# Kernel optimization log

Hardware: AMD Instinct MI355X
Metric: run time of the kernel (lower is better)

Reference implementation:

```python
import jax, jax.numpy as jnp
import numpy as np

B, S, D = 1, 2048, 4096
H, KVH, HD = 32, 8, 128


def setup_inputs() -> dict:
    key = jax.random.key(0)
    ks = jax.random.split(key, 6)
    x = jax.random.normal(ks[0], (B, S, D), dtype=jnp.float32)
    # Llama3 RoPE angles: theta = 500000
    inv_freq = 1.0 / (500000.0 ** (np.arange(0, HD, 2, dtype=np.float32) / HD))
    ang = np.arange(S, dtype=np.float32)[:, None] * inv_freq[None, :]  # [S, HD//2]
    freqs_cos = jnp.asarray(np.cos(ang), dtype=jnp.float32)
    freqs_sin = jnp.asarray(np.sin(ang), dtype=jnp.float32)
    sc = 0.02
    wq = jax.random.normal(ks[1], (H * HD, D), dtype=jnp.float32) * sc
    wk = jax.random.normal(ks[2], (KVH * HD, D), dtype=jnp.float32) * sc
    wv = jax.random.normal(ks[3], (KVH * HD, D), dtype=jnp.float32) * sc
    wo = jax.random.normal(ks[4], (D, H * HD), dtype=jnp.float32) * sc
    return {"x": x, "freqs_cos": freqs_cos, "freqs_sin": freqs_sin,
            "wq": wq, "wk": wk, "wv": wv, "wo": wo}


def _rope(t, cos, sin):
    # t: [B, S, h, HD]; rotate consecutive pairs (complex multiply)
    t2 = t.reshape(*t.shape[:-1], HD // 2, 2)
    x0, x1 = t2[..., 0], t2[..., 1]
    c = cos[None, :, None, :]
    s = sin[None, :, None, :]
    r0 = x0 * c - x1 * s
    r1 = x0 * s + x1 * c
    return jnp.stack([r0, r1], axis=-1).reshape(t.shape)


def reference(x, freqs_cos, freqs_sin, wq, wk, wv, wo):
    b, s, _ = x.shape
    q = jnp.einsum('bsd,ed->bse', x, wq).reshape(b, s, H, HD)
    k = jnp.einsum('bsd,ed->bse', x, wk).reshape(b, s, KVH, HD)
    v = jnp.einsum('bsd,ed->bse', x, wv).reshape(b, s, KVH, HD)
    q = _rope(q, freqs_cos, freqs_sin)
    k = _rope(k, freqs_cos, freqs_sin)
    # GQA: repeat kv heads
    rep = H // KVH
    k = jnp.repeat(k, rep, axis=2)
    v = jnp.repeat(v, rep, axis=2)
    scale = 1.0 / jnp.sqrt(jnp.asarray(HD, dtype=x.dtype))
    scores = jnp.einsum('bqhd,bkhd->bhqk', q, k) * scale
    causal = jnp.tril(jnp.ones((s, s), dtype=bool))
    scores = jnp.where(causal[None, None], scores, jnp.finfo(scores.dtype).min)
    p = jax.nn.softmax(scores, axis=-1)
    out = jnp.einsum('bhqk,bkhd->bqhd', p, v).reshape(b, s, H * HD)
    return jnp.einsum('bse,de->bsd', out, wo)
```

## Files before the change

### kernel.cpp

```cpp
#include <hip/hip_runtime.h>

typedef unsigned short u16;
typedef short bf16x8 __attribute__((ext_vector_type(8)));
typedef float f32x4 __attribute__((ext_vector_type(4)));

#define S_LEN 2048
#define ATT_SCALE 0.08838834764831845f
#define NEG_BIG  -1.0e30f

static __device__ __forceinline__ float bf2f(u16 u) {
  union { unsigned int i; float f; } v; v.i = ((unsigned int)u) << 16; return v.f;
}
static __device__ __forceinline__ u16 f2bf(float f) {
  union { float f; unsigned int i; } v; v.f = f;
  unsigned int x = v.i;
  return (u16)((x + 0x7fffu + ((x >> 16) & 1u)) >> 16);
}

static __device__ __forceinline__ void gl_lds16(const u16* g, u16* l) {
  __builtin_amdgcn_global_load_lds(
      (const __attribute__((address_space(1))) unsigned int*)g,
      (__attribute__((address_space(3))) unsigned int*)l, 16, 0, 0);
}

static __device__ __forceinline__ bf16x8 load8(const u16* p) { return *(const bf16x8*)p; }
static __device__ __forceinline__ bf16x8 load8(const float* p) {
  f32x4 a = *(const f32x4*)p;
  f32x4 b = *(const f32x4*)(p + 4);
  bf16x8 r;
  r[0] = (short)f2bf(a[0]); r[1] = (short)f2bf(a[1]);
  r[2] = (short)f2bf(a[2]); r[3] = (short)f2bf(a[3]);
  r[4] = (short)f2bf(b[0]); r[5] = (short)f2bf(b[1]);
  r[6] = (short)f2bf(b[2]); r[7] = (short)f2bf(b[3]);
  return r;
}
static __device__ __forceinline__ void store_out(u16* C, size_t i, float v)  { C[i] = f2bf(v); }
static __device__ __forceinline__ void store_out(float* C, size_t i, float v){ C[i] = v; }

__global__ __launch_bounds__(256) void f2b_kernel(
    const float* __restrict__ s, u16* __restrict__ d, int n8) {
  int i = blockIdx.x * 256 + threadIdx.x;
  if (i >= n8) return;
  *(bf16x8*)&d[(size_t)i * 8] = load8(s + (size_t)i * 8);
}

template <typename OT>
static __device__ __forceinline__ void gemm_core(
    const u16* __restrict__ A, const u16* __restrict__ B, OT* __restrict__ C,
    int K, int ldc, int bm, int bn) {
  __shared__ __align__(16) u16 As[128 * 64];
  __shared__ __align__(16) u16 Bs[128 * 64];
  const int tid  = threadIdx.x;
  const int lane = tid & 63;
  const int wave = tid >> 6;
  const int wm = (wave >> 1) << 6;
  const int wn = (wave & 1) << 6;
  const int col  = lane & 15;
  const int quad = lane >> 4;

  const f32x4 fzero = {0.f, 0.f, 0.f, 0.f};
  f32x4 acc[4][4];
#pragma unroll
  for (int i = 0; i < 4; ++i)
#pragma unroll
    for (int j = 0; j < 4; ++j) acc[i][j] = fzero;

  const int srow = (lane >> 3);
  const int sc8  = lane & 7;

  for (int k0 = 0; k0 < K; k0 += 64) {
#pragma unroll
    for (int i = 0; i < 4; ++i) {
      int r = wave * 32 + i * 8 + srow;
      int src = (sc8 ^ (r & 7)) << 3;
      gl_lds16(A + (size_t)(bm + r) * K + k0 + src, &As[(wave * 32 + i * 8) * 64]);
      gl_lds16(B + (size_t)(bn + r) * K + k0 + src, &Bs[(wave * 32 + i * 8) * 64]);
    }
    __syncthreads();
#pragma unroll
    for (int kk = 0; kk < 64; kk += 32) {
      bf16x8 af[4], bfr[4];
#pragma unroll
      for (int mt = 0; mt < 4; ++mt) {
        int row = wm + mt * 16 + col;
        af[mt] = *(const bf16x8*)&As[row * 64 + ((((kk >> 3) + quad) ^ (col & 7)) << 3)];
      }
#pragma unroll
      for (int nt = 0; nt < 4; ++nt) {
        int row = wn + nt * 16 + col;
        bfr[nt] = *(const bf16x8*)&Bs[row * 64 + ((((kk >> 3) + quad) ^ (col & 7)) << 3)];
      }
#pragma unroll
      for (int mt = 0; mt < 4; ++mt)
#pragma unroll
        for (int nt = 0; nt < 4; ++nt)
          acc[mt][nt] = __builtin_amdgcn_mfma_f32_16x16x32_bf16(
              af[mt], bfr[nt], acc[mt][nt], 0, 0, 0);
    }
    __syncthreads();
  }
#pragma unroll
  for (int mt = 0; mt < 4; ++mt)
#pragma unroll
    for (int nt = 0; nt < 4; ++nt)
#pragma unroll
      for (int r = 0; r < 4; ++r) {
        int row = bm + wm + mt * 16 + quad * 4 + r;
        int cn  = bn + wn + nt * 16 + col;
        store_out(C, (size_t)row * ldc + cn, acc[mt][nt][r]);
      }
}

__global__ __launch_bounds__(256) void gemm_qkv(
    const u16* __restrict__ xb, const u16* __restrict__ wqb,
    const u16* __restrict__ wkb, const u16* __restrict__ wvb,
    u16* __restrict__ q, u16* __restrict__ k, u16* __restrict__ v) {
  int bx = blockIdx.x;
  const u16* B; u16* C; int ldc, bn;
  if (bx < 32)      { B = wqb; C = q; ldc = 4096; bn = bx * 128; }
  else if (bx < 40) { B = wkb; C = k; ldc = 1024; bn = (bx - 32) * 128; }
  else              { B = wvb; C = v; ldc = 1024; bn = (bx - 40) * 128; }
  gemm_core<u16>(xb, B, C, 4096, ldc, blockIdx.y * 128, bn);
}

__global__ __launch_bounds__(256) void gemm_o(
    const u16* __restrict__ ao, const u16* __restrict__ wob, float* __restrict__ out) {
  gemm_core<float>(ao, wob, out, 4096, 4096, blockIdx.y * 128, blockIdx.x * 128);
}

#define LDK 72
template <typename AT, typename BT, typename OT>
__global__ __launch_bounds__(256) void gemm_bt(
    const AT* __restrict__ A, const BT* __restrict__ B,
    OT* __restrict__ C, int M, int N, int K) {
  __shared__ __align__(16) u16 As[128 * LDK];
  __shared__ __align__(16) u16 Bs[128 * LDK];
  const int tid  = threadIdx.x;
  const int lane = tid & 63;
  const int wave = tid >> 6;
  const int wm = (wave >> 1) << 6;
  const int wn = (wave & 1) << 6;
  const int col  = lane & 15;
  const int quad = lane >> 4;
  const int bm = blockIdx.y * 128;
  const int bn = blockIdx.x * 128;

  const f32x4 fzero = {0.f, 0.f, 0.f, 0.f};
  f32x4 acc[4][4];
#pragma unroll
  for (int i = 0; i < 4; ++i)
#pragma unroll
    for (int j = 0; j < 4; ++j) acc[i][j] = fzero;

  const int sr = tid >> 3;
  const int sc = (tid & 7) * 8;
  const AT* Aptr = A + (size_t)(bm + sr) * K + sc;
  const BT* Bptr = B + (size_t)(bn + sr) * K + sc;

  for (int k0 = 0; k0 < K; k0 += 64) {
#pragma unroll
    for (int p = 0; p < 4; ++p) {
      *(bf16x8*)&As[(sr + 32 * p) * LDK + sc] = load8(Aptr + (size_t)(32 * p) * K + k0);
      *(bf16x8*)&Bs[(sr + 32 * p) * LDK + sc] = load8(Bptr + (size_t)(32 * p) * K + k0);
    }
    __syncthreads();
#pragma unroll
    for (int kk = 0; kk < 64; kk += 32) {
      bf16x8 af[4], bfr[4];
#pragma unroll
      for (int mt = 0; mt < 4; ++mt)
        af[mt] = *(const bf16x8*)&As[(wm + mt * 16 + col) * LDK + kk + quad * 8];
#pragma unroll
      for (int nt = 0; nt < 4; ++nt)
        bfr[nt] = *(const bf16x8*)&Bs[(wn + nt * 16 + col) * LDK + kk + quad * 8];
#pragma unroll
      for (int mt = 0; mt < 4; ++mt)
#pragma unroll
        for (int nt = 0; nt < 4; ++nt)
          acc[mt][nt] = __builtin_amdgcn_mfma_f32_16x16x32_bf16(
              af[mt], bfr[nt], acc[mt][nt], 0, 0, 0);
    }
    __syncthreads();
  }
#pragma unroll
  for (int mt = 0; mt < 4; ++mt)
#pragma unroll
    for (int nt = 0; nt < 4; ++nt)
#pragma unroll
      for (int r = 0; r < 4; ++r) {
        int row = bm + wm + mt * 16 + quad * 4 + r;
        int cn  = bn + wn + nt * 16 + col;
        store_out(C, (size_t)row * N + cn, acc[mt][nt][r]);
      }
}

__global__ __launch_bounds__(256) void rope_kernel(
    u16* __restrict__ q, u16* __restrict__ k,
    const float* __restrict__ cs, const float* __restrict__ sn) {
  int idx = blockIdx.x * 256 + threadIdx.x;
  const int QP = S_LEN * 32 * 64;
  u16* base;
  int s, i;
  bool isq = idx < QP;
  if (isq) {
    s = idx >> 11; int w = idx & 2047; i = w & 63;
    base = q + (size_t)s * 4096 + (w >> 6) * 128 + 2 * i;
  } else {
    int j = idx - QP;
    s = j >> 9; int w = j & 511; i = w & 63;
    base = k + (size_t)s * 1024 + (w >> 6) * 128 + 2 * i;
  }
  float c  = cs[s * 64 + i];
  float sv = sn[s * 64 + i];
  float x0 = bf2f(base[0]);
  float x1 = bf2f(base[1]);
  float r0 = x0 * c - x1 * sv;
  float r1 = x0 * sv + x1 * c;
  if (isq) { r0 *= ATT_SCALE; r1 *= ATT_SCALE; }
  base[0] = f2bf(r0);
  base[1] = f2bf(r1);
}

__global__ __launch_bounds__(256, 3) void attn_kernel(
    const u16* __restrict__ Q, const u16* __restrict__ K,
    const u16* __restrict__ V, u16* __restrict__ O) {
  const int qb   = 31 - blockIdx.x;
  const int h    = blockIdx.y;
  const int kvh  = h >> 2;
  const int tid  = threadIdx.x;
  const int lane = tid & 63;
  const int wave = tid >> 6;
  const int col  = lane & 15;
  const int quad = lane >> 4;

  __shared__ __align__(16) u16 Ks[64 * 128];
  __shared__ __align__(16) u16 Vt[128 * 64];

  const int qpos = qb * 64 + wave * 16 + col;

  bf16x8 qf[4];
#pragma unroll
  for (int kb = 0; kb < 4; ++kb)
    qf[kb] = *(const bf16x8*)&Q[(size_t)qpos * 4096 + h * 128 + kb * 32 + quad * 8];

  const f32x4 fzero = {0.f, 0.f, 0.f, 0.f};
  f32x4 oacc[8];
#pragma unroll
  for (int nt = 0; nt < 8; ++nt) oacc[nt] = fzero;
  float m_ = NEG_BIG, l_ = 0.f;

  const int krow = lane >> 4;
  const int kcnk = lane & 15;
  const int vsc  = (tid & 15) * 8;
  const int vrp  = tid >> 4;
  const int vrot = tid & 7;

  const int nchunk = qb + 1;
  for (int c = 0; c < nchunk; ++c) {
    const int pos0 = c * 64;
#pragma unroll
    for (int i = 0; i < 4; ++i) {
      int r = wave * 16 + i * 4 + krow;
      int src = ((kcnk & 8) | ((kcnk ^ r) & 7)) << 3;
      gl_lds16(&K[(size_t)(pos0 + r) * 1024 + kvh * 128 + src],
               &Ks[(wave * 16 + i * 4) * 128]);
    }
#pragma unroll
    for (int it = 0; it < 2; ++it) {
      int rp = vrp + it * 16;
      const u16* vp = &V[(size_t)(pos0 + 2 * rp) * 1024 + kvh * 128 + vsc];
      union { bf16x8 v; u16 u[8]; } ue, uo;
      ue.v = *(const bf16x8*)vp;
      uo.v = *(const bf16x8*)(vp + 1024);
      int pc = rp >> 2, pi = rp & 3;
#pragma unroll
      for (int j = 0; j < 8; ++j) {
        int jj = (j + vrot) & 7;
        int hd = vsc + jj;
        unsigned val = (unsigned)ue.u[jj] | ((unsigned)uo.u[jj] << 16);
        *(unsigned*)&Vt[hd * 64 + ((pc ^ (hd & 7)) << 3) + pi * 2] = val;
      }
    }
    __syncthreads();

    f32x4 sv[4];
#pragma unroll
    for (int kv = 0; kv < 4; ++kv) sv[kv] = fzero;
#pragma unroll
    for (int kv = 0; kv < 4; ++kv) {
      int r = kv * 16 + col;
#pragma unroll
      for (int kb = 0; kb < 4; ++kb) {
        int kq = kb * 4 + quad;
        int slot = (kq & 8) | ((kq ^ r) & 7);
        bf16x8 kf = *(const bf16x8*)&Ks[r * 128 + slot * 8];
        sv[kv] = __builtin_amdgcn_mfma_f32_16x16x32_bf16(kf, qf[kb], sv[kv], 0, 0, 0);
      }
    }

    float mx = NEG_BIG;
#pragma unroll
    for (int kv = 0; kv < 4; ++kv)
#pragma unroll
      for (int r = 0; r < 4; ++r) {
        float s = (pos0 + kv * 16 + quad * 4 + r) <= qpos ? sv[kv][r] : NEG_BIG;
        sv[kv][r] = s;
        mx = fmaxf(mx, s);
      }
    mx = fmaxf(mx, __shfl_xor(mx, 16));
    mx = fmaxf(mx, __shfl_xor(mx, 32));
    float mnew  = fmaxf(m_, mx);
    float alpha = __expf(m_ - mnew);
    float ls = 0.f;
#pragma unroll
    for (int kv = 0; kv < 4; ++kv)
#pragma unroll
      for (int r = 0; r < 4; ++r) {
        float p = __expf(sv[kv][r] - mnew);
        sv[kv][r] = p;
        ls += p;
      }
    ls += __shfl_xor(ls, 16);
    ls += __shfl_xor(ls, 32);
    l_ = l_ * alpha + ls;
    m_ = mnew;
#pragma unroll
    for (int nt = 0; nt < 8; ++nt) {
      oacc[nt][0] *= alpha; oacc[nt][1] *= alpha;
      oacc[nt][2] *= alpha; oacc[nt][3] *= alpha;
    }

    unsigned pk[4][2];
#pragma unroll
    for (int kv = 0; kv < 4; ++kv) {
      pk[kv][0] = (unsigned)f2bf(sv[kv][0]) | ((unsigned)f2bf(sv[kv][1]) << 16);
      pk[kv][1] = (unsigned)f2bf(sv[kv][2]) | ((unsigned)f2bf(sv[kv][3]) << 16);
    }

    const int idxA = col + 16 * (2 * (quad & 1));
    const int idxB = idxA + 16;
    const bool hi  = quad >= 2;
#pragma unroll
    for (int kc = 0; kc < 2; ++kc) {
      unsigned a00 = __shfl(pk[2 * kc][0],     idxA);
      unsigned a01 = __shfl(pk[2 * kc][1],     idxA);
      unsigned a10 = __shfl(pk[2 * kc + 1][0], idxA);
      unsigned a11 = __shfl(pk[2 * kc + 1][1], idxA);
      unsigned b00 = __shfl(pk[2 * kc][0],     idxB);
      unsigned b01 = __shfl(pk[2 * kc][1],     idxB);
      unsigned b10 = __shfl(pk[2 * kc + 1][0], idxB);
      unsigned b11 = __shfl(pk[2 * kc + 1][1], idxB);
      union { unsigned u[4]; bf16x8 v; } pb;
      pb.u[0] = hi ? a10 : a00;
      pb.u[1] = hi ? a11 : a01;
      pb.u[2] = hi ? b10 : b00;
      pb.u[3] = hi ? b11 : b01;
#pragma unroll
      for (int nt = 0; nt < 8; ++nt) {
        int hd = nt * 16 + col;
        int pc = kc * 4 + quad;
        bf16x8 vf = *(const bf16x8*)&Vt[hd * 64 + ((pc ^ (hd & 7)) << 3)];
        oacc[nt] = __builtin_amdgcn_mfma_f32_16x16x32_bf16(vf, pb.v, oacc[nt], 0, 0, 0);
      }
    }
    __syncthreads();
  }

  float inv = 1.f / l_;
#pragma unroll
  for (int nt = 0; nt < 8; ++nt) {
    union { u16 u[4]; unsigned long long ll; } w;
    w.u[0] = f2bf(oacc[nt][0] * inv);
    w.u[1] = f2bf(oacc[nt][1] * inv);
    w.u[2] = f2bf(oacc[nt][2] * inv);
    w.u[3] = f2bf(oacc[nt][3] * inv);
    *(unsigned long long*)&O[(size_t)qpos * 4096 + h * 128 + nt * 16 + quad * 4] = w.ll;
  }
}

extern "C" void kernel_launch(void* const* d_in, const int* in_sizes, int n_in,
                              void* d_out, int out_size, void* d_ws, size_t ws_size,
                              hipStream_t stream) {
  const float* x  = (const float*)d_in[0];
  const float* fc = (const float*)d_in[1];
  const float* fs = (const float*)d_in[2];
  const float* wq = (const float*)d_in[3];
  const float* wk = (const float*)d_in[4];
  const float* wv = (const float*)d_in[5];
  const float* wo = (const float*)d_in[6];
  float* out = (float*)d_out;

  u16* q  = (u16*)d_ws;
  u16* k  = q + (size_t)8388608;
  u16* v  = k + (size_t)2097152;
  u16* ao = v + (size_t)2097152;

  dim3 blk(256, 1, 1);
  const size_t NEED_FAST = 109051904ULL;

  if (ws_size >= NEED_FAST) {
    u16* xb  = ao  + (size_t)8388608;
    u16* wqb = xb  + (size_t)8388608;
    u16* wkb = wqb + (size_t)16777216;
    u16* wvb = wkb + (size_t)4194304;
    u16* wob = wqb;

    hipLaunchKernelGGL(f2b_kernel, dim3(4096, 1, 1), blk, 0, stream, x,  xb,  1048576);
    hipLaunchKernelGGL(f2b_kernel, dim3(8192, 1, 1), blk, 0, stream, wq, wqb, 2097152);
    hipLaunchKernelGGL(f2b_kernel, dim3(2048, 1, 1), blk, 0, stream, wk, wkb, 524288);
    hipLaunchKernelGGL(f2b_kernel, dim3(2048, 1, 1), blk, 0, stream, wv, wvb, 524288);
    hipLaunchKernelGGL(gemm_qkv, dim3(48, 16, 1), blk, 0, stream, xb, wqb, wkb, wvb, q, k, v);
    hipLaunchKernelGGL(f2b_kernel, dim3(8192, 1, 1), blk, 0, stream, wo, wob, 2097152);
    hipLaunchKernelGGL(rope_kernel, dim3(20480, 1, 1), blk, 0, stream, q, k, fc, fs);
    hipLaunchKernelGGL(attn_kernel, dim3(32, 32, 1), blk, 0, stream, q, k, v, ao);
    hipLaunchKernelGGL(gemm_o, dim3(32, 16, 1), blk, 0, stream, ao, wob, out);
  } else {
    hipLaunchKernelGGL((gemm_bt<float, float, u16>), dim3(32, 16, 1), blk, 0, stream,
                       x, wq, q, 2048, 4096, 4096);
    hipLaunchKernelGGL((gemm_bt<float, float, u16>), dim3(8, 16, 1),  blk, 0, stream,
                       x, wk, k, 2048, 1024, 4096);
    hipLaunchKernelGGL((gemm_bt<float, float, u16>), dim3(8, 16, 1),  blk, 0, stream,
                       x, wv, v, 2048, 1024, 4096);
    hipLaunchKernelGGL(rope_kernel, dim3(20480, 1, 1), blk, 0, stream, q, k, fc, fs);
    hipLaunchKernelGGL(attn_kernel, dim3(32, 32, 1), blk, 0, stream, q, k, v, ao);
    hipLaunchKernelGGL((gemm_bt<u16, float, float>), dim3(32, 16, 1), blk, 0, stream,
                       ao, wo, out, 2048, 4096, 4096);
  }
}
```

Measured before the change: 668.8 us.

## Pair complementary causal query blocks per attention workgroup to balance load

Each attention workgroup now processes two query blocks, ib and 31-ib, sharing the loaded K/V tiles across both. This balances causal-triangle work across workgroups, since every block does about 33 chunks, and halves K/V reloads for the shorter block. The grid is halved to 512 workgroups and the launch bounds drop to 2 waves per SIMD, because register pressure doubles from the two accumulator sets. That lowers occupancy and parallelism.

```diff
diff --git a/kernel.cpp b/kernel.cpp
--- a/kernel.cpp
+++ b/kernel.cpp
@@ -221,10 +221,12 @@
   base[1] = f2bf(r1);
 }
 
-__global__ __launch_bounds__(256, 3) void attn_kernel(
+__global__ __launch_bounds__(256, 2) void attn_kernel(
     const u16* __restrict__ Q, const u16* __restrict__ K,
     const u16* __restrict__ V, u16* __restrict__ O) {
-  const int qb   = 31 - blockIdx.x;
+  const int ib   = blockIdx.x;
+  const int qbA  = ib;
+  const int qbB  = 31 - ib;
   const int h    = blockIdx.y;
   const int kvh  = h >> 2;
   const int tid  = threadIdx.x;
@@ -236,18 +238,21 @@
   __shared__ __align__(16) u16 Ks[64 * 128];
   __shared__ __align__(16) u16 Vt[128 * 64];
 
-  const int qpos = qb * 64 + wave * 16 + col;
-
-  bf16x8 qf[4];
-#pragma unroll
-  for (int kb = 0; kb < 4; ++kb)
-    qf[kb] = *(const bf16x8*)&Q[(size_t)qpos * 4096 + h * 128 + kb * 32 + quad * 8];
+  const int qposA = qbA * 64 + wave * 16 + col;
+  const int qposB = qbB * 64 + wave * 16 + col;
+
+  bf16x8 qfA[4], qfB[4];
+#pragma unroll
+  for (int kb = 0; kb < 4; ++kb) {
+    qfA[kb] = *(const bf16x8*)&Q[(size_t)qposA * 4096 + h * 128 + kb * 32 + quad * 8];
+    qfB[kb] = *(const bf16x8*)&Q[(size_t)qposB * 4096 + h * 128 + kb * 32 + quad * 8];
+  }
 
   const f32x4 fzero = {0.f, 0.f, 0.f, 0.f};
-  f32x4 oacc[8];
-#pragma unroll
-  for (int nt = 0; nt < 8; ++nt) oacc[nt] = fzero;
-  float m_ = NEG_BIG, l_ = 0.f;
+  f32x4 oaccA[8], oaccB[8];
+#pragma unroll
+  for (int nt = 0; nt < 8; ++nt) { oaccA[nt] = fzero; oaccB[nt] = fzero; }
+  float mA = NEG_BIG, lA = 0.f, mB = NEG_BIG, lB = 0.f;
 
   const int krow = lane >> 4;
   const int kcnk = lane & 15;
@@ -255,34 +260,10 @@
   const int vrp  = tid >> 4;
   const int vrot = tid & 7;
 
-  const int nchunk = qb + 1;
-  for (int c = 0; c < nchunk; ++c) {
-    const int pos0 = c * 64;
-#pragma unroll
-    for (int i = 0; i < 4; ++i) {
-      int r = wave * 16 + i * 4 + krow;
-      int src = ((kcnk & 8) | ((kcnk ^ r) & 7)) << 3;
-      gl_lds16(&K[(size_t)(pos0 + r) * 1024 + kvh * 128 + src],
-               &Ks[(wave * 16 + i * 4) * 128]);
-    }
-#pragma unroll
-    for (int it = 0; it < 2; ++it) {
-      int rp = vrp + it * 16;
-      const u16* vp = &V[(size_t)(pos0 + 2 * rp) * 1024 + kvh * 128 + vsc];
-      union { bf16x8 v; u16 u[8]; } ue, uo;
-      ue.v = *(const bf16x8*)vp;
-      uo.v = *(const bf16x8*)(vp + 1024);
-      int pc = rp >> 2, pi = rp & 3;
-#pragma unroll
-      for (int j = 0; j < 8; ++j) {
-        int jj = (j + vrot) & 7;
-        int hd = vsc + jj;
-        unsigned val = (unsigned)ue.u[jj] | ((unsigned)uo.u[jj] << 16);
-        *(unsigned*)&Vt[hd * 64 + ((pc ^ (hd & 7)) << 3) + pi * 2] = val;
-      }
-    }
-    __syncthreads();
-
+  int pos0 = 0;
+
+  auto tile_step = [&](const bf16x8* qf, f32x4* oacc, float& m_, float& l_,
+                       int qpos) {
     f32x4 sv[4];
 #pragma unroll
     for (int kv = 0; kv < 4; ++kv) sv[kv] = fzero;
@@ -363,18 +344,58 @@
         oacc[nt] = __builtin_amdgcn_mfma_f32_16x16x32_bf16(vf, pb.v, oacc[nt], 0, 0, 0);
       }
     }
-    __syncthreads();
-  }
-
-  float inv = 1.f / l_;
+  };
+
+  const int nchunk = qbB + 1;
+  for (int c = 0; c < nchunk; ++c) {
+    pos0 = c * 64;
+#pragma unroll
+    for (int i = 0; i < 4; ++i) {
+      int r = wave * 16 + i * 4 + krow;
+      int src = ((kcnk & 8) | ((kcnk ^ r) & 7)) << 3;
+      gl_lds16(&K[(size_t)(pos0 + r) * 1024 + kvh * 128 + src],
+               &Ks[(wave * 16 + i * 4) * 128]);
+    }
+#pragma unroll
+    for (int it = 0; it < 2; ++it) {
+      int rp = vrp + it * 16;
+      const u16* vp = &V[(size_t)(pos0 + 2 * rp) * 1024 + kvh * 128 + vsc];
+      union { bf16x8 v; u16 u[8]; } ue, uo;
+      ue.v = *(const bf16x8*)vp;
+      uo.v = *(const bf16x8*)(vp + 1024);
+      int pc = rp >> 2, pi = rp & 3;
+#pragma unroll
+      for (int j = 0; j < 8; ++j) {
+        int jj = (j + vrot) & 7;
+        int hd = vsc + jj;
+        unsigned val = (unsigned)ue.u[jj] | ((unsigned)uo.u[jj] << 16);
+        *(unsigned*)&Vt[hd * 64 + ((pc ^ (hd & 7)) << 3) + pi * 2] = val;
+      }
+    }
+    __syncthreads();
+
+    tile_step(qfB, oaccB, mB, lB, qposB);
+    if (c <= qbA)
+      tile_step(qfA, oaccA, mA, lA, qposA);
+
+    __syncthreads();
+  }
+
+  float invA = 1.f / lA;
+  float invB = 1.f / lB;
 #pragma unroll
   for (int nt = 0; nt < 8; ++nt) {
-    union { u16 u[4]; unsigned long long ll; } w;
-    w.u[0] = f2bf(oacc[nt][0] * inv);
-    w.u[1] = f2bf(oacc[nt][1] * inv);
-    w.u[2] = f2bf(oacc[nt][2] * inv);
-    w.u[3] = f2bf(oacc[nt][3] * inv);
-    *(unsigned long long*)&O[(size_t)qpos * 4096 + h * 128 + nt * 16 + quad * 4] = w.ll;
+    union { u16 u[4]; unsigned long long ll; } wA, wB;
+    wA.u[0] = f2bf(oaccA[nt][0] * invA);
+    wA.u[1] = f2bf(oaccA[nt][1] * invA);
+    wA.u[2] = f2bf(oaccA[nt][2] * invA);
+    wA.u[3] = f2bf(oaccA[nt][3] * invA);
+    wB.u[0] = f2bf(oaccB[nt][0] * invB);
+    wB.u[1] = f2bf(oaccB[nt][1] * invB);
+    wB.u[2] = f2bf(oaccB[nt][2] * invB);
+    wB.u[3] = f2bf(oaccB[nt][3] * invB);
+    *(unsigned long long*)&O[(size_t)qposA * 4096 + h * 128 + nt * 16 + quad * 4] = wA.ll;
+    *(unsigned long long*)&O[(size_t)qposB * 4096 + h * 128 + nt * 16 + quad * 4] = wB.ll;
   }
 }
 
@@ -412,7 +433,7 @@
     hipLaunchKernelGGL(gemm_qkv, dim3(48, 16, 1), blk, 0, stream, xb, wqb, wkb, wvb, q, k, v);
     hipLaunchKernelGGL(f2b_kernel, dim3(8192, 1, 1), blk, 0, stream, wo, wob, 2097152);
     hipLaunchKernelGGL(rope_kernel, dim3(20480, 1, 1), blk, 0, stream, q, k, fc, fs);
-    hipLaunchKernelGGL(attn_kernel, dim3(32, 32, 1), blk, 0, stream, q, k, v, ao);
+    hipLaunchKernelGGL(attn_kernel, dim3(16, 32, 1), blk, 0, stream, q, k, v, ao);
     hipLaunchKernelGGL(gemm_o, dim3(32, 16, 1), blk, 0, stream, ao, wob, out);
   } else {
     hipLaunchKernelGGL((gemm_bt<float, float, u16>), dim3(32, 16, 1), blk, 0, stream,
@@ -422,7 +443,7 @@
     hipLaunchKernelGGL((gemm_bt<float, float, u16>), dim3(8, 16, 1),  blk, 0, stream,
                        x, wv, v, 2048, 1024, 4096);
     hipLaunchKernelGGL(rope_kernel, dim3(20480, 1, 1), blk, 0, stream, q, k, fc, fs);
-    hipLaunchKernelGGL(attn_kernel, dim3(32, 32, 1), blk, 0, stream, q, k, v, ao);
+    hipLaunchKernelGGL(attn_kernel, dim3(16, 32, 1), blk, 0, stream, q, k, v, ao);
     hipLaunchKernelGGL((gemm_bt<u16, float, float>), dim3(32, 16, 1), blk, 0, stream,
                        ao, wo, out, 2048, 4096, 4096);
   }
```

Result: slower. 805.8 us (+20.5%).

## Double-buffer K/V tiles and pair causal query blocks per workgroup

Applied to the files above, without the earlier changes.

The attention kernel now gives each workgroup two query blocks (ib and 31-ib) to balance causal work, and halves the grid to 16x32. K/V tiles are double-buffered in shared memory. The next chunk's K is loaded asynchronously and its V is held in registers and written to LDS after the current chunk's compute, which hides global load latency behind the MFMA work. Occupancy drops from 3 to 2 blocks per CU because of the doubled LDS and extra registers, and the grid has only 512 blocks, which may underfill the GPU.

```diff
diff --git a/kernel.cpp b/kernel.cpp
--- a/kernel.cpp
+++ b/kernel.cpp
@@ -221,10 +221,10 @@
   base[1] = f2bf(r1);
 }
 
-__global__ __launch_bounds__(256, 3) void attn_kernel(
+__global__ __launch_bounds__(256, 2) void attn_kernel(
     const u16* __restrict__ Q, const u16* __restrict__ K,
     const u16* __restrict__ V, u16* __restrict__ O) {
-  const int qb   = 31 - blockIdx.x;
+  const int ib   = blockIdx.x;
   const int h    = blockIdx.y;
   const int kvh  = h >> 2;
   const int tid  = threadIdx.x;
@@ -233,21 +233,10 @@
   const int col  = lane & 15;
   const int quad = lane >> 4;
 
-  __shared__ __align__(16) u16 Ks[64 * 128];
-  __shared__ __align__(16) u16 Vt[128 * 64];
-
-  const int qpos = qb * 64 + wave * 16 + col;
-
-  bf16x8 qf[4];
-#pragma unroll
-  for (int kb = 0; kb < 4; ++kb)
-    qf[kb] = *(const bf16x8*)&Q[(size_t)qpos * 4096 + h * 128 + kb * 32 + quad * 8];
+  __shared__ __align__(16) u16 Ks[2][64 * 128];
+  __shared__ __align__(16) u16 Vt[2][128 * 64];
 
   const f32x4 fzero = {0.f, 0.f, 0.f, 0.f};
-  f32x4 oacc[8];
-#pragma unroll
-  for (int nt = 0; nt < 8; ++nt) oacc[nt] = fzero;
-  float m_ = NEG_BIG, l_ = 0.f;
 
   const int krow = lane >> 4;
   const int kcnk = lane & 15;
@@ -255,126 +244,169 @@
   const int vrp  = tid >> 4;
   const int vrot = tid & 7;
 
-  const int nchunk = qb + 1;
-  for (int c = 0; c < nchunk; ++c) {
+  bf16x8 ve[2], vo[2];
+
+  auto stage_load = [&](int c, int buf) {
     const int pos0 = c * 64;
+    u16* Kb = Ks[buf];
 #pragma unroll
     for (int i = 0; i < 4; ++i) {
       int r = wave * 16 + i * 4 + krow;
       int src = ((kcnk & 8) | ((kcnk ^ r) & 7)) << 3;
       gl_lds16(&K[(size_t)(pos0 + r) * 1024 + kvh * 128 + src],
-               &Ks[(wave * 16 + i * 4) * 128]);
+               &Kb[(wave * 16 + i * 4) * 128]);
     }
 #pragma unroll
     for (int it = 0; it < 2; ++it) {
       int rp = vrp + it * 16;
       const u16* vp = &V[(size_t)(pos0 + 2 * rp) * 1024 + kvh * 128 + vsc];
+      ve[it] = *(const bf16x8*)vp;
+      vo[it] = *(const bf16x8*)(vp + 1024);
+    }
+  };
+
+  auto stage_write = [&](int buf) {
+    u16* Vb = Vt[buf];
+#pragma unroll
+    for (int it = 0; it < 2; ++it) {
+      int rp = vrp + it * 16;
       union { bf16x8 v; u16 u[8]; } ue, uo;
-      ue.v = *(const bf16x8*)vp;
-      uo.v = *(const bf16x8*)(vp + 1024);
+      ue.v = ve[it]; uo.v = vo[it];
       int pc = rp >> 2, pi = rp & 3;
 #pragma unroll
       for (int j = 0; j < 8; ++j) {
         int jj = (j + vrot) & 7;
         int hd = vsc + jj;
         unsigned val = (unsigned)ue.u[jj] | ((unsigned)uo.u[jj] << 16);
-        *(unsigned*)&Vt[hd * 64 + ((pc ^ (hd & 7)) << 3) + pi * 2] = val;
-      }
-    }
+        *(unsigned*)&Vb[hd * 64 + ((pc ^ (hd & 7)) << 3) + pi * 2] = val;
+      }
+    }
+  };
+
+  for (int t = 0; t < 2; ++t) {
+    const int qb   = t ? 31 - ib : ib;
+    const int qpos = qb * 64 + wave * 16 + col;
+
+    bf16x8 qf[4];
+#pragma unroll
+    for (int kb = 0; kb < 4; ++kb)
+      qf[kb] = *(const bf16x8*)&Q[(size_t)qpos * 4096 + h * 128 + kb * 32 + quad * 8];
+
+    f32x4 oacc[8];
+#pragma unroll
+    for (int nt = 0; nt < 8; ++nt) oacc[nt] = fzero;
+    float m_ = NEG_BIG, l_ = 0.f;
+
+    const int nchunk = qb + 1;
+    int cur = 0;
+    stage_load(0, 0);
+    stage_write(0);
     __syncthreads();
 
-    f32x4 sv[4];
-#pragma unroll
-    for (int kv = 0; kv < 4; ++kv) sv[kv] = fzero;
-#pragma unroll
-    for (int kv = 0; kv < 4; ++kv) {
-      int r = kv * 16 + col;
-#pragma unroll
-      for (int kb = 0; kb < 4; ++kb) {
-        int kq = kb * 4 + quad;
-        int slot = (kq & 8) | ((kq ^ r) & 7);
-        bf16x8 kf = *(const bf16x8*)&Ks[r * 128 + slot * 8];
-        sv[kv] = __builtin_amdgcn_mfma_f32_16x16x32_bf16(kf, qf[kb], sv[kv], 0, 0, 0);
-      }
-    }
-
-    float mx = NEG_BIG;
-#pragma unroll
-    for (int kv = 0; kv < 4; ++kv)
-#pragma unroll
-      for (int r = 0; r < 4; ++r) {
-        float s = (pos0 + kv * 16 + quad * 4 + r) <= qpos ? sv[kv][r] : NEG_BIG;
-        sv[kv][r] = s;
-        mx = fmaxf(mx, s);
-      }
-    mx = fmaxf(mx, __shfl_xor(mx, 16));
-    mx = fmaxf(mx, __shfl_xor(mx, 32));
-    float mnew  = fmaxf(m_, mx);
-    float alpha = __expf(m_ - mnew);
-    float ls = 0.f;
-#pragma unroll
-    for (int kv = 0; kv < 4; ++kv)
-#pragma unroll
-      for (int r = 0; r < 4; ++r) {
-        float p = __expf(sv[kv][r] - mnew);
-        sv[kv][r] = p;
-        ls += p;
-      }
-    ls += __shfl_xor(ls, 16);
-    ls += __shfl_xor(ls, 32);
-    l_ = l_ * alpha + ls;
-    m_ = mnew;
+    for (int c = 0; c < nchunk; ++c) {
+      const int pos0 = c * 64;
+      const bool pf = (c + 1 < nchunk);
+      if (pf) stage_load(c + 1, cur ^ 1);
+
+      const u16* Kb = Ks[cur];
+      const u16* Vb = Vt[cur];
+
+      f32x4 sv[4];
+#pragma unroll
+      for (int kv = 0; kv < 4; ++kv) sv[kv] = fzero;
+#pragma unroll
+      for (int kv = 0; kv < 4; ++kv) {
+        int r = kv * 16 + col;
+#pragma unroll
+        for (int kb = 0; kb < 4; ++kb) {
+          int kq = kb * 4 + quad;
+          int slot = (kq & 8) | ((kq ^ r) & 7);
+          bf16x8 kf = *(const bf16x8*)&Kb[r * 128 + slot * 8];
+          sv[kv] = __builtin_amdgcn_mfma_f32_16x16x32_bf16(kf, qf[kb], sv[kv], 0, 0, 0);
+        }
+      }
+
+      float mx = NEG_BIG;
+#pragma unroll
+      for (int kv = 0; kv < 4; ++kv)
+#pragma unroll
+        for (int r = 0; r < 4; ++r) {
+          float s = (pos0 + kv * 16 + quad * 4 + r) <= qpos ? sv[kv][r] : NEG_BIG;
+          sv[kv][r] = s;
+          mx = fmaxf(mx, s);
+        }
+      mx = fmaxf(mx, __shfl_xor(mx, 16));
+      mx = fmaxf(mx, __shfl_xor(mx, 32));
+      float mnew  = fmaxf(m_, mx);
+      float alpha = __expf(m_ - mnew);
+      float ls = 0.f;
+#pragma unroll
+      for (int kv = 0; kv < 4; ++kv)
+#pragma unroll
+        for (int r = 0; r < 4; ++r) {
+          float p = __expf(sv[kv][r] - mnew);
+          sv[kv][r] = p;
+          ls += p;
+        }
+      ls += __shfl_xor(ls, 16);
+      ls += __shfl_xor(ls, 32);
+      l_ = l_ * alpha + ls;
+      m_ = mnew;
+#pragma unroll
+      for (int nt = 0; nt < 8; ++nt) {
+        oacc[nt][0] *= alpha; oacc[nt][1] *= alpha;
+        oacc[nt][2] *= alpha; oacc[nt][3] *= alpha;
+      }
+
+      unsigned pk[4][2];
+#pragma unroll
+      for (int kv = 0; kv < 4; ++kv) {
+        pk[kv][0] = (unsigned)f2bf(sv[kv][0]) | ((unsigned)f2bf(sv[kv][1]) << 16);
+        pk[kv][1] = (unsigned)f2bf(sv[kv][2]) | ((unsigned)f2bf(sv[kv][3]) << 16);
+      }
+
+      const int idxA = col + 16 * (2 * (quad & 1));
+      const int idxB = idxA + 16;
+      const bool hi  = quad >= 2;
+#pragma unroll
+      for (int kc = 0; kc < 2; ++kc) {
+        unsigned a00 = __shfl(pk[2 * kc][0],     idxA);
+        unsigned a01 = __shfl(pk[2 * kc][1],     idxA);
+        unsigned a10 = __shfl(pk[2 * kc + 1][0], idxA);
+        unsigned a11 = __shfl(pk[2 * kc + 1][1], idxA);
+        unsigned b00 = __shfl(pk[2 * kc][0],     idxB);
+        unsigned b01 = __shfl(pk[2 * kc][1],     idxB);
+        unsigned b10 = __shfl(pk[2 * kc + 1][0], idxB);
+        unsigned b11 = __shfl(pk[2 * kc + 1][1], idxB);
+        union { unsigned u[4]; bf16x8 v; } pb;
+        pb.u[0] = hi ? a10 : a00;
+        pb.u[1] = hi ? a11 : a01;
+        pb.u[2] = hi ? b10 : b00;
+        pb.u[3] = hi ? b11 : b01;
+#pragma unroll
+        for (int nt = 0; nt < 8; ++nt) {
+          int hd = nt * 16 + col;
+          int pc = kc * 4 + quad;
+          bf16x8 vf = *(const bf16x8*)&Vb[hd * 64 + ((pc ^ (hd & 7)) << 3)];
+          oacc[nt] = __builtin_amdgcn_mfma_f32_16x16x32_bf16(vf, pb.v, oacc[nt], 0, 0, 0);
+        }
+      }
+
+      if (pf) stage_write(cur ^ 1);
+      __syncthreads();
+      cur ^= 1;
+    }
+
+    float inv = 1.f / l_;
 #pragma unroll
     for (int nt = 0; nt < 8; ++nt) {
-      oacc[nt][0] *= alpha; oacc[nt][1] *= alpha;
-      oacc[nt][2] *= alpha; oacc[nt][3] *= alpha;
-    }
-
-    unsigned pk[4][2];
-#pragma unroll
-    for (int kv = 0; kv < 4; ++kv) {
-      pk[kv][0] = (unsigned)f2bf(sv[kv][0]) | ((unsigned)f2bf(sv[kv][1]) << 16);
-      pk[kv][1] = (unsigned)f2bf(sv[kv][2]) | ((unsigned)f2bf(sv[kv][3]) << 16);
-    }
-
-    const int idxA = col + 16 * (2 * (quad & 1));
-    const int idxB = idxA + 16;
-    const bool hi  = quad >= 2;
-#pragma unroll
-    for (int kc = 0; kc < 2; ++kc) {
-      unsigned a00 = __shfl(pk[2 * kc][0],     idxA);
-      unsigned a01 = __shfl(pk[2 * kc][1],     idxA);
-      unsigned a10 = __shfl(pk[2 * kc + 1][0], idxA);
-      unsigned a11 = __shfl(pk[2 * kc + 1][1], idxA);
-      unsigned b00 = __shfl(pk[2 * kc][0],     idxB);
-      unsigned b01 = __shfl(pk[2 * kc][1],     idxB);
-      unsigned b10 = __shfl(pk[2 * kc + 1][0], idxB);
-      unsigned b11 = __shfl(pk[2 * kc + 1][1], idxB);
-      union { unsigned u[4]; bf16x8 v; } pb;
-      pb.u[0] = hi ? a10 : a00;
-      pb.u[1] = hi ? a11 : a01;
-      pb.u[2] = hi ? b10 : b00;
-      pb.u[3] = hi ? b11 : b01;
-#pragma unroll
-      for (int nt = 0; nt < 8; ++nt) {
-        int hd = nt * 16 + col;
-        int pc = kc * 4 + quad;
-        bf16x8 vf = *(const bf16x8*)&Vt[hd * 64 + ((pc ^ (hd & 7)) << 3)];
-        oacc[nt] = __builtin_amdgcn_mfma_f32_16x16x32_bf16(vf, pb.v, oacc[nt], 0, 0, 0);
-      }
-    }
-    __syncthreads();
-  }
-
-  float inv = 1.f / l_;
-#pragma unroll
-  for (int nt = 0; nt < 8; ++nt) {
-    union { u16 u[4]; unsigned long long ll; } w;
-    w.u[0] = f2bf(oacc[nt][0] * inv);
-    w.u[1] = f2bf(oacc[nt][1] * inv);
-    w.u[2] = f2bf(oacc[nt][2] * inv);
-    w.u[3] = f2bf(oacc[nt][3] * inv);
-    *(unsigned long long*)&O[(size_t)qpos * 4096 + h * 128 + nt * 16 + quad * 4] = w.ll;
+      union { u16 u[4]; unsigned long long ll; } w;
+      w.u[0] = f2bf(oacc[nt][0] * inv);
+      w.u[1] = f2bf(oacc[nt][1] * inv);
+      w.u[2] = f2bf(oacc[nt][2] * inv);
+      w.u[3] = f2bf(oacc[nt][3] * inv);
+      *(unsigned long long*)&O[(size_t)qpos * 4096 + h * 128 + nt * 16 + quad * 4] = w.ll;
+    }
   }
 }
 
@@ -412,7 +444,7 @@
     hipLaunchKernelGGL(gemm_qkv, dim3(48, 16, 1), blk, 0, stream, xb, wqb, wkb, wvb, q, k, v);
     hipLaunchKernelGGL(f2b_kernel, dim3(8192, 1, 1), blk, 0, stream, wo, wob, 2097152);
     hipLaunchKernelGGL(rope_kernel, dim3(20480, 1, 1), blk, 0, stream, q, k, fc, fs);
-    hipLaunchKernelGGL(attn_kernel, dim3(32, 32, 1), blk, 0, stream, q, k, v, ao);
+    hipLaunchKernelGGL(attn_kernel, dim3(16, 32, 1), blk, 0, stream, q, k, v, ao);
     hipLaunchKernelGGL(gemm_o, dim3(32, 16, 1), blk, 0, stream, ao, wob, out);
   } else {
     hipLaunchKernelGGL((gemm_bt<float, float, u16>), dim3(32, 16, 1), blk, 0, stream,
@@ -422,7 +454,7 @@
     hipLaunchKernelGGL((gemm_bt<float, float, u16>), dim3(8, 16, 1),  blk, 0, stream,
                        x, wv, v, 2048, 1024, 4096);
     hipLaunchKernelGGL(rope_kernel, dim3(20480, 1, 1), blk, 0, stream, q, k, fc, fs);
-    hipLaunchKernelGGL(attn_kernel, dim3(32, 32, 1), blk, 0, stream, q, k, v, ao);
+    hipLaunchKernelGGL(attn_kernel, dim3(16, 32, 1), blk, 0, stream, q, k, v, ao);
     hipLaunchKernelGGL((gemm_bt<u16, float, float>), dim3(32, 16, 1), blk, 0, stream,
                        ao, wo, out, 2048, 4096, 4096);
   }
```

After: 554.2 us. 17.1% less time.

## Split attention KV range across two wave groups with paired causal query blocks

Applied to the files above, without the earlier changes.

The attention kernel now uses 512-thread blocks. Each block handles two query blocks, ib and 31-ib, so the causal work per block is balanced. For each query block, two 4-wave groups process the two halves of the KV chunks and merge their partial softmax states through LDS. It also moves to exp2 with log2e folded into the Q scale, skips causal masking off the diagonal, skips the rescale when the max grows by no more than 8, and sets MFMA priority. The costs are extra LDS and a merge step per query block, and the lazy-rescale threshold trades some numerical headroom.

```diff
diff --git a/kernel.cpp b/kernel.cpp
--- a/kernel.cpp
+++ b/kernel.cpp
@@ -5,7 +5,7 @@
 typedef float f32x4 __attribute__((ext_vector_type(4)));
 
 #define S_LEN 2048
-#define ATT_SCALE 0.08838834764831845f
+#define ATT_SCALE (0.08838834764831845f * 1.4426950408889634f)
 #define NEG_BIG  -1.0e30f
 
 static __device__ __forceinline__ float bf2f(u16 u) {
@@ -15,6 +15,9 @@
   union { float f; unsigned int i; } v; v.f = f;
   unsigned int x = v.i;
   return (u16)((x + 0x7fffu + ((x >> 16) & 1u)) >> 16);
+}
+static __device__ __forceinline__ float fexp2(float x) {
+  return __builtin_amdgcn_exp2f(x);
 }
 
 static __device__ __forceinline__ void gl_lds16(const u16* g, u16* l) {
@@ -221,160 +224,212 @@
   base[1] = f2bf(r1);
 }
 
-__global__ __launch_bounds__(256, 3) void attn_kernel(
+__global__ __launch_bounds__(512, 4) void attn_kernel(
     const u16* __restrict__ Q, const u16* __restrict__ K,
     const u16* __restrict__ V, u16* __restrict__ O) {
-  const int qb   = 31 - blockIdx.x;
+  const int ib   = blockIdx.x;
   const int h    = blockIdx.y;
   const int kvh  = h >> 2;
   const int tid  = threadIdx.x;
   const int lane = tid & 63;
   const int wave = tid >> 6;
+  const int grp  = wave >> 2;
+  const int wl   = wave & 3;
   const int col  = lane & 15;
   const int quad = lane >> 4;
-
-  __shared__ __align__(16) u16 Ks[64 * 128];
-  __shared__ __align__(16) u16 Vt[128 * 64];
-
-  const int qpos = qb * 64 + wave * 16 + col;
-
-  bf16x8 qf[4];
-#pragma unroll
-  for (int kb = 0; kb < 4; ++kb)
-    qf[kb] = *(const bf16x8*)&Q[(size_t)qpos * 4096 + h * 128 + kb * 32 + quad * 8];
+  const int gt   = tid & 255;
+
+  __shared__ __align__(16) u16 SMEM[2][16384];
+  u16* Kb = &SMEM[grp][0];
+  u16* Vb = &SMEM[grp][8192];
 
   const f32x4 fzero = {0.f, 0.f, 0.f, 0.f};
-  f32x4 oacc[8];
-#pragma unroll
-  for (int nt = 0; nt < 8; ++nt) oacc[nt] = fzero;
-  float m_ = NEG_BIG, l_ = 0.f;
 
   const int krow = lane >> 4;
   const int kcnk = lane & 15;
-  const int vsc  = (tid & 15) * 8;
-  const int vrp  = tid >> 4;
-  const int vrot = tid & 7;
-
-  const int nchunk = qb + 1;
-  for (int c = 0; c < nchunk; ++c) {
-    const int pos0 = c * 64;
-#pragma unroll
-    for (int i = 0; i < 4; ++i) {
-      int r = wave * 16 + i * 4 + krow;
-      int src = ((kcnk & 8) | ((kcnk ^ r) & 7)) << 3;
-      gl_lds16(&K[(size_t)(pos0 + r) * 1024 + kvh * 128 + src],
-               &Ks[(wave * 16 + i * 4) * 128]);
-    }
-#pragma unroll
-    for (int it = 0; it < 2; ++it) {
-      int rp = vrp + it * 16;
-      const u16* vp = &V[(size_t)(pos0 + 2 * rp) * 1024 + kvh * 128 + vsc];
-      union { bf16x8 v; u16 u[8]; } ue, uo;
-      ue.v = *(const bf16x8*)vp;
-      uo.v = *(const bf16x8*)(vp + 1024);
-      int pc = rp >> 2, pi = rp & 3;
-#pragma unroll
-      for (int j = 0; j < 8; ++j) {
-        int jj = (j + vrot) & 7;
-        int hd = vsc + jj;
-        unsigned val = (unsigned)ue.u[jj] | ((unsigned)uo.u[jj] << 16);
-        *(unsigned*)&Vt[hd * 64 + ((pc ^ (hd & 7)) << 3) + pi * 2] = val;
-      }
-    }
-    __syncthreads();
-
-    f32x4 sv[4];
-#pragma unroll
-    for (int kv = 0; kv < 4; ++kv) sv[kv] = fzero;
-#pragma unroll
-    for (int kv = 0; kv < 4; ++kv) {
-      int r = kv * 16 + col;
-#pragma unroll
-      for (int kb = 0; kb < 4; ++kb) {
-        int kq = kb * 4 + quad;
-        int slot = (kq & 8) | ((kq ^ r) & 7);
-        bf16x8 kf = *(const bf16x8*)&Ks[r * 128 + slot * 8];
-        sv[kv] = __builtin_amdgcn_mfma_f32_16x16x32_bf16(kf, qf[kb], sv[kv], 0, 0, 0);
-      }
-    }
-
-    float mx = NEG_BIG;
-#pragma unroll
-    for (int kv = 0; kv < 4; ++kv)
-#pragma unroll
-      for (int r = 0; r < 4; ++r) {
-        float s = (pos0 + kv * 16 + quad * 4 + r) <= qpos ? sv[kv][r] : NEG_BIG;
-        sv[kv][r] = s;
-        mx = fmaxf(mx, s);
-      }
-    mx = fmaxf(mx, __shfl_xor(mx, 16));
-    mx = fmaxf(mx, __shfl_xor(mx, 32));
-    float mnew  = fmaxf(m_, mx);
-    float alpha = __expf(m_ - mnew);
-    float ls = 0.f;
-#pragma unroll
-    for (int kv = 0; kv < 4; ++kv)
-#pragma unroll
-      for (int r = 0; r < 4; ++r) {
-        float p = __expf(sv[kv][r] - mnew);
-        sv[kv][r] = p;
-        ls += p;
-      }
-    ls += __shfl_xor(ls, 16);
-    ls += __shfl_xor(ls, 32);
-    l_ = l_ * alpha + ls;
-    m_ = mnew;
-#pragma unroll
-    for (int nt = 0; nt < 8; ++nt) {
-      oacc[nt][0] *= alpha; oacc[nt][1] *= alpha;
-      oacc[nt][2] *= alpha; oacc[nt][3] *= alpha;
-    }
-
-    unsigned pk[4][2];
-#pragma unroll
-    for (int kv = 0; kv < 4; ++kv) {
-      pk[kv][0] = (unsigned)f2bf(sv[kv][0]) | ((unsigned)f2bf(sv[kv][1]) << 16);
-      pk[kv][1] = (unsigned)f2bf(sv[kv][2]) | ((unsigned)f2bf(sv[kv][3]) << 16);
-    }
-
-    const int idxA = col + 16 * (2 * (quad & 1));
-    const int idxB = idxA + 16;
-    const bool hi  = quad >= 2;
-#pragma unroll
-    for (int kc = 0; kc < 2; ++kc) {
-      unsigned a00 = __shfl(pk[2 * kc][0],     idxA);
-      unsigned a01 = __shfl(pk[2 * kc][1],     idxA);
-      unsigned a10 = __shfl(pk[2 * kc + 1][0], idxA);
-      unsigned a11 = __shfl(pk[2 * kc + 1][1], idxA);
-      unsigned b00 = __shfl(pk[2 * kc][0],     idxB);
-      unsigned b01 = __shfl(pk[2 * kc][1],     idxB);
-      unsigned b10 = __shfl(pk[2 * kc + 1][0], idxB);
-      unsigned b11 = __shfl(pk[2 * kc + 1][1], idxB);
-      union { unsigned u[4]; bf16x8 v; } pb;
-      pb.u[0] = hi ? a10 : a00;
-      pb.u[1] = hi ? a11 : a01;
-      pb.u[2] = hi ? b10 : b00;
-      pb.u[3] = hi ? b11 : b01;
+  const int vsc  = (gt & 15) * 8;
+  const int vrp  = gt >> 4;
+  const int vrot = gt & 7;
+
+  for (int t = 0; t < 2; ++t) {
+    const int qb   = t ? 31 - ib : ib;
+    const int qpos = qb * 64 + wl * 16 + col;
+    const int ql   = wl * 16 + col;
+
+    bf16x8 qf[4];
+#pragma unroll
+    for (int kb = 0; kb < 4; ++kb)
+      qf[kb] = *(const bf16x8*)&Q[(size_t)qpos * 4096 + h * 128 + kb * 32 + quad * 8];
+
+    f32x4 oacc[8];
+#pragma unroll
+    for (int nt = 0; nt < 8; ++nt) oacc[nt] = fzero;
+    float m_ = NEG_BIG, l_ = 0.f;
+
+    const int n  = qb + 1;
+    const int h0 = (n + 1) >> 1;
+    const int c0 = grp ? h0 : 0;
+    const int c1 = grp ? n  : h0;
+
+    for (int rnd = 0; rnd < h0; ++rnd) {
+      const int c = c0 + rnd;
+      const bool act = c < c1;
+      if (act) {
+        const int pos0 = c * 64;
+#pragma unroll
+        for (int i = 0; i < 4; ++i) {
+          int r = wl * 16 + i * 4 + krow;
+          int src = ((kcnk & 8) | ((kcnk ^ r) & 7)) << 3;
+          gl_lds16(&K[(size_t)(pos0 + r) * 1024 + kvh * 128 + src],
+                   &Kb[(wl * 16 + i * 4) * 128]);
+        }
+#pragma unroll
+        for (int it = 0; it < 2; ++it) {
+          int rp = vrp + it * 16;
+          const u16* vp = &V[(size_t)(pos0 + 2 * rp) * 1024 + kvh * 128 + vsc];
+          union { bf16x8 v; u16 u[8]; } ue, uo;
+          ue.v = *(const bf16x8*)vp;
+          uo.v = *(const bf16x8*)(vp + 1024);
+          int pc = rp >> 2, pi = rp & 3;
+#pragma unroll
+          for (int j = 0; j < 8; ++j) {
+            int jj = (j + vrot) & 7;
+            int hd = vsc + jj;
+            unsigned val = (unsigned)ue.u[jj] | ((unsigned)uo.u[jj] << 16);
+            *(unsigned*)&Vb[hd * 64 + ((pc ^ (hd & 7)) << 3) + pi * 2] = val;
+          }
+        }
+      }
+      __syncthreads();
+      if (act) {
+        const int pos0 = c * 64;
+        const bool diag = (c == qb);
+
+        f32x4 sv[4];
+#pragma unroll
+        for (int kv = 0; kv < 4; ++kv) sv[kv] = fzero;
+        __builtin_amdgcn_s_setprio(1);
+#pragma unroll
+        for (int kv = 0; kv < 4; ++kv) {
+          int r = kv * 16 + col;
+#pragma unroll
+          for (int kb = 0; kb < 4; ++kb) {
+            int kq = kb * 4 + quad;
+            int slot = (kq & 8) | ((kq ^ r) & 7);
+            bf16x8 kf = *(const bf16x8*)&Kb[r * 128 + slot * 8];
+            sv[kv] = __builtin_amdgcn_mfma_f32_16x16x32_bf16(kf, qf[kb], sv[kv], 0, 0, 0);
+          }
+        }
+        __builtin_amdgcn_s_setprio(0);
+
+        float mx = NEG_BIG;
+        if (diag) {
+#pragma unroll
+          for (int kv = 0; kv < 4; ++kv)
+#pragma unroll
+            for (int r = 0; r < 4; ++r) {
+              float s = (pos0 + kv * 16 + quad * 4 + r) <= qpos ? sv[kv][r] : NEG_BIG;
+              sv[kv][r] = s;
+              mx = fmaxf(mx, s);
+            }
+        } else {
+#pragma unroll
+          for (int kv = 0; kv < 4; ++kv)
+#pragma unroll
+            for (int r = 0; r < 4; ++r) mx = fmaxf(mx, sv[kv][r]);
+        }
+        mx = fmaxf(mx, __shfl_xor(mx, 16));
+        mx = fmaxf(mx, __shfl_xor(mx, 32));
+        if (!__all(mx - m_ <= 8.f)) {
+          float mnew  = fmaxf(m_, mx);
+          float alpha = fexp2(m_ - mnew);
+          l_ *= alpha;
+#pragma unroll
+          for (int nt = 0; nt < 8; ++nt) {
+            oacc[nt][0] *= alpha; oacc[nt][1] *= alpha;
+            oacc[nt][2] *= alpha; oacc[nt][3] *= alpha;
+          }
+          m_ = mnew;
+        }
+        float ls = 0.f;
+#pragma unroll
+        for (int kv = 0; kv < 4; ++kv)
+#pragma unroll
+          for (int r = 0; r < 4; ++r) {
+            float p = fexp2(sv[kv][r] - m_);
+            sv[kv][r] = p;
+            ls += p;
+          }
+        ls += __shfl_xor(ls, 16);
+        ls += __shfl_xor(ls, 32);
+        l_ += ls;
+
+        unsigned pk[4][2];
+#pragma unroll
+        for (int kv = 0; kv < 4; ++kv) {
+          pk[kv][0] = (unsigned)f2bf(sv[kv][0]) | ((unsigned)f2bf(sv[kv][1]) << 16);
+          pk[kv][1] = (unsigned)f2bf(sv[kv][2]) | ((unsigned)f2bf(sv[kv][3]) << 16);
+        }
+
+        const int idxA = col + 16 * (2 * (quad & 1));
+        const int idxB = idxA + 16;
+        const bool hi  = quad >= 2;
+#pragma unroll
+        for (int kc = 0; kc < 2; ++kc) {
+          unsigned a00 = __shfl(pk[2 * kc][0],     idxA);
+          unsigned a01 = __shfl(pk[2 * kc][1],     idxA);
+          unsigned a10 = __shfl(pk[2 * kc + 1][0], idxA);
+          unsigned a11 = __shfl(pk[2 * kc + 1][1], idxA);
+          unsigned b00 = __shfl(pk[2 * kc][0],     idxB);
+          unsigned b01 = __shfl(pk[2 * kc][1],     idxB);
+          unsigned b10 = __shfl(pk[2 * kc + 1][0], idxB);
+          unsigned b11 = __shfl(pk[2 * kc + 1][1], idxB);
+          union { unsigned u[4]; bf16x8 v; } pb;
+          pb.u[0] = hi ? a10 : a00;
+          pb.u[1] = hi ? a11 : a01;
+          pb.u[2] = hi ? b10 : b00;
+          pb.u[3] = hi ? b11 : b01;
+          __builtin_amdgcn_s_setprio(1);
+#pragma unroll
+          for (int nt = 0; nt < 8; ++nt) {
+            int hd = nt * 16 + col;
+            int pc = kc * 4 + quad;
+            bf16x8 vf = *(const bf16x8*)&Vb[hd * 64 + ((pc ^ (hd & 7)) << 3)];
+            oacc[nt] = __builtin_amdgcn_mfma_f32_16x16x32_bf16(vf, pb.v, oacc[nt], 0, 0, 0);
+          }
+          __builtin_amdgcn_s_setprio(0);
+        }
+      }
+      __syncthreads();
+    }
+
+    float* MF = (float*)&SMEM[0][0];
+    float* ML = MF + 64 * 132;
+    if (grp == 1) {
+#pragma unroll
+      for (int nt = 0; nt < 8; ++nt)
+        *(f32x4*)&MF[ql * 132 + nt * 16 + quad * 4] = oacc[nt];
+      if (quad == 0) { ML[2 * ql] = m_; ML[2 * ql + 1] = l_; }
+    }
+    __syncthreads();
+    if (grp == 0) {
+      float m1 = ML[2 * ql], l1 = ML[2 * ql + 1];
+      float mn = fmaxf(m_, m1);
+      float a0 = fexp2(m_ - mn), a1 = fexp2(m1 - mn);
+      float li = 1.f / (l_ * a0 + l1 * a1);
+      a0 *= li; a1 *= li;
 #pragma unroll
       for (int nt = 0; nt < 8; ++nt) {
-        int hd = nt * 16 + col;
-        int pc = kc * 4 + quad;
-        bf16x8 vf = *(const bf16x8*)&Vt[hd * 64 + ((pc ^ (hd & 7)) << 3)];
-        oacc[nt] = __builtin_amdgcn_mfma_f32_16x16x32_bf16(vf, pb.v, oacc[nt], 0, 0, 0);
-      }
-    }
-    __syncthreads();
-  }
-
-  float inv = 1.f / l_;
-#pragma unroll
-  for (int nt = 0; nt < 8; ++nt) {
-    union { u16 u[4]; unsigned long long ll; } w;
-    w.u[0] = f2bf(oacc[nt][0] * inv);
-    w.u[1] = f2bf(oacc[nt][1] * inv);
-    w.u[2] = f2bf(oacc[nt][2] * inv);
-    w.u[3] = f2bf(oacc[nt][3] * inv);
-    *(unsigned long long*)&O[(size_t)qpos * 4096 + h * 128 + nt * 16 + quad * 4] = w.ll;
+        f32x4 o1 = *(const f32x4*)&MF[ql * 132 + nt * 16 + quad * 4];
+        union { u16 u[4]; unsigned long long ll; } w;
+        w.u[0] = f2bf(oacc[nt][0] * a0 + o1[0] * a1);
+        w.u[1] = f2bf(oacc[nt][1] * a0 + o1[1] * a1);
+        w.u[2] = f2bf(oacc[nt][2] * a0 + o1[2] * a1);
+        w.u[3] = f2bf(oacc[nt][3] * a0 + o1[3] * a1);
+        *(unsigned long long*)&O[(size_t)qpos * 4096 + h * 128 + nt * 16 + quad * 4] = w.ll;
+      }
+    }
+    __syncthreads();
   }
 }
 
@@ -396,6 +451,7 @@
   u16* ao = v + (size_t)2097152;
 
   dim3 blk(256, 1, 1);
+  dim3 ablk(512, 1, 1);
   const size_t NEED_FAST = 109051904ULL;
 
   if (ws_size >= NEED_FAST) {
@@ -412,7 +468,7 @@
     hipLaunchKernelGGL(gemm_qkv, dim3(48, 16, 1), blk, 0, stream, xb, wqb, wkb, wvb, q, k, v);
     hipLaunchKernelGGL(f2b_kernel, dim3(8192, 1, 1), blk, 0, stream, wo, wob, 2097152);
     hipLaunchKernelGGL(rope_kernel, dim3(20480, 1, 1), blk, 0, stream, q, k, fc, fs);
-    hipLaunchKernelGGL(attn_kernel, dim3(32, 32, 1), blk, 0, stream, q, k, v, ao);
+    hipLaunchKernelGGL(attn_kernel, dim3(16, 32, 1), ablk, 0, stream, q, k, v, ao);
     hipLaunchKernelGGL(gemm_o, dim3(32, 16, 1), blk, 0, stream, ao, wob, out);
   } else {
     hipLaunchKernelGGL((gemm_bt<float, float, u16>), dim3(32, 16, 1), blk, 0, stream,
@@ -422,7 +478,7 @@
     hipLaunchKernelGGL((gemm_bt<float, float, u16>), dim3(8, 16, 1),  blk, 0, stream,
                        x, wv, v, 2048, 1024, 4096);
     hipLaunchKernelGGL(rope_kernel, dim3(20480, 1, 1), blk, 0, stream, q, k, fc, fs);
-    hipLaunchKernelGGL(attn_kernel, dim3(32, 32, 1), blk, 0, stream, q, k, v, ao);
+    hipLaunchKernelGGL(attn_kernel, dim3(16, 32, 1), ablk, 0, stream, q, k, v, ao);
     hipLaunchKernelGGL((gemm_bt<u16, float, float>), dim3(32, 16, 1), blk, 0, stream,
                        ao, wo, out, 2048, 4096, 4096);
   }
```

New measurement: 542.4 us. 1.23x faster.
